# Performance work log

Measured on AMD Instinct MI355X. Metric: run time of the kernel, lower is better.

Reference implementation:

```python
import jax, jax.numpy as jnp
import numpy as np

O, NI, F, D, NN, M = 2048, 16, 4, 128, 8, 8  # outfits, item slots, factors, dim, neighbors, valid slots
D2 = D // 2

def lrelu(x):
    return jax.nn.leaky_relu(x, 0.01)

def mlp2(x, W1, b1, W2, b2):
    # Linear -> LeakyReLU -> Linear -> LeakyReLU (Dropout is identity at inference)
    return lrelu(lrelu(x @ W1 + b1) @ W2 + b2)

def setup_inputs():
    ks = jax.random.split(jax.random.key(0), 16)
    s = 0.05
    pos = jnp.arange(NI)[None, :]
    outfit_items = jnp.where(pos < M, jax.random.randint(ks[0], (O, NI), 0, NI), -1)
    items_neighbor = jax.random.randint(ks[1], (O, NI, NN), -1, NI)
    items_feature = jax.random.normal(ks[2], (O, NI, D), dtype=jnp.float32)
    items_factors = jnp.zeros((O, NI, F, D), dtype=jnp.float32)
    p = {
        'cf_W1': jax.random.normal(ks[3], (F, D, D2)) * s,
        'cf_b1': jnp.zeros((F, D2)),
        'cf_W2': jax.random.normal(ks[4], (F, D2, D)) * s,
        'cf_b2': jnp.zeros((F, D)),
        'f2f_W1': jax.random.normal(ks[5], (D, D)) * s, 'f2f_b1': jnp.zeros((D,)),
        'f2f_W2': jax.random.normal(ks[6], (D, D)) * s, 'f2f_b2': jnp.zeros((D,)),
        'f2i_W1': jax.random.normal(ks[7], (D, D)) * s, 'f2i_b1': jnp.zeros((D,)),
        'f2i_W2': jax.random.normal(ks[8], (D, D)) * s, 'f2i_b2': jnp.zeros((D,)),
        'i2i_W1': jax.random.normal(ks[9], (D, D)) * s, 'i2i_b1': jnp.zeros((D,)),
        'i2i_W2': jax.random.normal(ks[10], (D, D)) * s, 'i2i_b2': jnp.zeros((D,)),
        'o2s_W': jax.random.normal(ks[11], (D, 1)) * s, 'o2s_b': jnp.zeros((1,)),
    }
    return dict(outfit_items=outfit_items, items_feature=items_feature,
                items_neighbor=items_neighbor, items_factors=items_factors, **p)

def _forward(outfit_items, items_feature, items_neighbor, items_factors,
             cf_W1, cf_b1, cf_W2, cf_b2, f2f_W1, f2f_b1, f2f_W2, f2f_b2,
             f2i_W1, f2i_b1, f2i_W2, f2i_b2, i2i_W1, i2i_b1, i2i_W2, i2i_b2,
             o2s_W, o2s_b):
    del items_factors  # creat_factors overwrites every entry in the original
    # --- creat_factors: per-factor 2-layer MLP on every item feature -> [O,NI,F,D]
    h = lrelu(jnp.einsum('oid,fde->oife', items_feature, cf_W1) + cf_b1)
    fac = lrelu(jnp.einsum('oife,fed->oifd', h, cf_W2) + cf_b2)

    # --- inter_factors: sequential over outfit slots; later slots read updated factors
    def outfit_fac(fac_o, oi_o, nbr_o):
        def step(f, i):
            valid = i != -1
            ic = jnp.maximum(i, 0)
            cand = jnp.concatenate([oi_o, nbr_o[ic]])                # [NI+NN]
            cm = (cand != -1) & (cand != i) & valid
            t = f[ic]                                                # [F,D] snapshot
            msg = mlp2(t[None] * f[jnp.maximum(cand, 0)],
                       f2f_W1, f2f_b1, f2f_W2, f2f_b2)               # [NI+NN,F,D]
            add = jnp.sum(jnp.where(cm[:, None, None], msg, 0.0), axis=0)
            return f.at[ic].add(jnp.where(valid, add, 0.0)), None
        f, _ = jax.lax.scan(step, fac_o, oi_o)
        return f
    fac = jax.vmap(outfit_fac)(fac, outfit_items, items_neighbor)

    # --- infer_items: feature[i] += sum_j f2i(fac[i,j]) for outfit members
    g = mlp2(fac, f2i_W1, f2i_b1, f2i_W2, f2i_b2).sum(axis=2)        # [O,NI,D]
    ic = jnp.maximum(outfit_items, 0)
    w = (outfit_items != -1).astype(g.dtype)                          # [O,NI]
    gsel = jnp.take_along_axis(g, ic[..., None], axis=1)
    scat = jax.vmap(lambda gs, idx, ww: jnp.zeros((NI, D), gs.dtype).at[idx].add(ww[:, None] * gs))
    feat = items_feature + scat(gsel, ic, w)

    # --- inter_items: sequential; current value detached (.data in original)
    def outfit_feat(fo_init, oi_o):
        jc = jnp.maximum(oi_o, 0)
        def step(fo, i):
            valid = i != -1
            ic_ = jnp.maximum(i, 0)
            t = jax.lax.stop_gradient(fo[ic_])
            msgs = mlp2(fo[jc], i2i_W1, i2i_b1, i2i_W2, i2i_b2)      # [NI,D]
            m = ((oi_o != -1) & (oi_o != i)).astype(fo.dtype)
            new = t + jnp.sum(m[:, None] * msgs, axis=0)
            return jnp.where(valid, fo.at[ic_].set(new), fo), None
        fo, _ = jax.lax.scan(step, fo_init, oi_o)
        return fo
    feat = jax.vmap(outfit_feat)(feat, outfit_items)

    # --- infer_outfit + score
    fsel = jnp.take_along_axis(feat, ic[..., None], axis=1)
    outfits = jnp.sum(w[..., None] * fsel, axis=1)                    # [O,D]
    scores = jax.nn.sigmoid(outfits @ o2s_W + o2s_b)[:, 0]            # [O]

    # --- com_loss: ||F F^T - I||_F^2 over valid slots (positional mask), / n_outfits
    G = jnp.einsum('oifd,oigd->oifg', fac, fac) - jnp.eye(F, dtype=fac.dtype)
    com = jnp.sum(w * jnp.sum(G * G, axis=(-1, -2))) / O
    return scores, jnp.reshape(com, (1,))

def reference(outfit_items, items_feature, items_neighbor, items_factors,
              cf_W1, cf_b1, cf_W2, cf_b2, f2f_W1, f2f_b1, f2f_W2, f2f_b2,
              f2i_W1, f2i_b1, f2i_W2, f2i_b2, i2i_W1, i2i_b1, i2i_W2, i2i_b2,
              o2s_W, o2s_b):
    return _forward(outfit_items, items_feature, items_neighbor, items_factors,
                    cf_W1, cf_b1, cf_W2, cf_b2, f2f_W1, f2f_b1, f2f_W2, f2f_b2,
                    f2i_W1, f2i_b1, f2i_W2, f2i_b2, i2i_W1, i2i_b1, i2i_W2, i2i_b2,
                    o2s_W, o2s_b)
```

## Files before the change

### kernel.cpp

```cpp
#include <hip/hip_runtime.h>
#include <hip/hip_bf16.h>
#include <math.h>


typedef __attribute__((ext_vector_type(8))) short short8;
typedef __attribute__((ext_vector_type(4))) float f32x4;

#define MFMA16(a, b, c) __builtin_amdgcn_mfma_f32_16x16x32_bf16(a, b, c, 0, 0, 0)

__device__ __forceinline__ float lrelu(float x) { return fmaxf(x, 0.01f * x); }

__device__ __forceinline__ ushort f2bf(float f) {
  unsigned u = __builtin_bit_cast(unsigned, f);
  u += 0x7fffu + ((u >> 16) & 1u);
  return (ushort)(u >> 16);
}
__device__ __forceinline__ float bflo(unsigned u) {
  return __builtin_bit_cast(float, u << 16);
}
__device__ __forceinline__ unsigned pk2(float a, float b) {
  float2 t; t.x = a; t.y = b;
  __hip_bfloat162 h = __float22bfloat162_rn(t);
  unsigned u;
  __builtin_memcpy(&u, &h, 4);
  return u;
}


__global__ __launch_bounds__(256) void prep_weights(
    const float* __restrict__ cfW1, const float* __restrict__ cfW2,
    const float* __restrict__ f2fW1, const float* __restrict__ f2fW2,
    const float* __restrict__ f2iW1, const float* __restrict__ f2iW2,
    const float* __restrict__ i2iW1, const float* __restrict__ i2iW2,
    ushort* __restrict__ ws, float* __restrict__ out) {
  const int idx = (int)(blockIdx.x * 256 + threadIdx.x);
  if (idx == 0) out[2048] = 0.0f;
  float v;
  if (idx < 32768) {
    int f = idx >> 13, r = idx & 8191, n = r >> 7, k = r & 127;
    v = cfW1[f * 8192 + k * 64 + n];
  } else if (idx < 65536) {
    int t = idx - 32768;
    int f = t >> 13, r = t & 8191, n = r >> 6, k = r & 63;
    v = cfW2[f * 8192 + k * 128 + n];
  } else {
    int t = idx - 65536;
    int seg = t >> 14, r = t & 16383, n = r >> 7, k = r & 127;
    const float* W = (seg == 0) ? f2fW1 : (seg == 1) ? f2fW2 :
                     (seg == 2) ? f2iW1 : (seg == 3) ? f2iW2 :
                     (seg == 4) ? i2iW1 : i2iW2;
    v = W[k * 128 + n];
  }
  ws[idx] = f2bf(v);
}

__global__ __launch_bounds__(512, 2) void mfgn_kernel(
    const int* __restrict__ outfit_items,
    const float* __restrict__ items_feature,
    const int* __restrict__ items_neighbor,
    const float* __restrict__ cfb1, const float* __restrict__ cfb2,
    const float* __restrict__ f2fb1, const float* __restrict__ f2fb2,
    const float* __restrict__ f2ib1, const float* __restrict__ f2ib2,
    const float* __restrict__ i2ib1, const float* __restrict__ i2ib2,
    const float* __restrict__ o2sW, const float* __restrict__ o2sb,
    const ushort* __restrict__ wsW,
    float* __restrict__ out)
{
  __shared__ float facL[16 * 540];
  __shared__ ushort prodS[8192] __attribute__((aligned(16)));
  __shared__ ushort hidS[8192] __attribute__((aligned(16)));
  __shared__ ushort featB[2048] __attribute__((aligned(16)));
  __shared__ float redE[8];
  __shared__ int oiL[16];
  __shared__ int clAll[256];
  __shared__ int ncAll[16];
  __shared__ int vslL[16];
  __shared__ int refcntL[16];
  __shared__ int nvsL;

  const int o = blockIdx.x;
  const int tid = (int)threadIdx.x;
  const int lane = tid & 63;
  const int wid = tid >> 6;
  const int n16 = lane & 15;
  const int q = lane >> 4;
  const int kb = q * 8;
  const int col = wid * 16 + n16;
  const int lx = lane * 8;
  const int fS = lane & 3, ciS = lane >> 2;
  const int kc0 = wid * 16;
  const int q0 = (wid & 1) * 2;
  const int sWA = ((wid >> 1) * 4 + (lane >> 4)) * 512 + (lane & 15) * 8;
  const int hwB = (wid >> 1) * 2048 + ((wid & 1) * 2 + (q >> 1)) * 128 + n16 * 8 + (q & 1) * 4;
  const int fbCol = (col >> 5) * 512 + ((col >> 3) & 3) * 128 + (col & 7);

  if (tid < 16) oiL[tid] = outfit_items[o * 16 + tid];
  {
    const int n = tid >> 5, d0 = (tid & 31) * 4;
    float4 v = *(const float4*)(items_feature + o * 2048 + tid * 4);
    uint2 pk; pk.x = pk2(v.x, v.y); pk.y = pk2(v.z, v.w);
    *(uint2*)(featB + (d0 >> 5) * 512 + (((d0 >> 3) & 3) * 16 + n) * 8 + (d0 & 7)) = pk;
  }
  if (tid == 0) {
    int cnt = 0;
    for (int s = 0; s < 16; ++s) refcntL[s] = 0;
    for (int s = 0; s < 16; ++s) {
      int v = oiL[s];
      if (v != -1) { vslL[cnt++] = s; refcntL[v]++; }
    }
    nvsL = cnt;
  }
  for (int s = wid; s < 16; s += 8) {
    const int iv = outfit_items[o * 16 + s];
    if (iv == -1) { if (lane == 0) ncAll[s] = 0; continue; }
    int cand = -1;
    if (lane < 24) cand = (lane < 16) ? outfit_items[o * 16 + lane]
                                      : items_neighbor[o * 128 + iv * 8 + (lane - 16)];
    bool ok = (lane < 24) && (cand != -1) && (cand != iv);
    unsigned long long bm = __ballot(ok);
    if (ok) clAll[s * 16 + __popcll(bm & ((1ull << lane) - 1ull))] = cand;
    if (lane == 0) ncAll[s] = (int)__popcll(bm);
  }
  __syncthreads();
  const int nvs = nvsL;

  {
    const int f = wid & 3, half = wid >> 2;
    short8 wA[2][4];
#pragma unroll
    for (int etl = 0; etl < 2; ++etl)
#pragma unroll
      for (int kt = 0; kt < 4; ++kt)
        wA[etl][kt] = *(const short8*)(wsW + (f * 64 + (half * 2 + etl) * 16 + n16) * 128
                                       + kt * 32 + kb);
    f32x4 acc[2];
#pragma unroll
    for (int etl = 0; etl < 2; ++etl)
      acc[etl] = *(const f32x4*)(cfb1 + f * 64 + (half * 2 + etl) * 16 + q * 4);
    __builtin_amdgcn_s_setprio(1);
    for (int kt = 0; kt < 4; ++kt) {
      short8 x = *(const short8*)(featB + kt * 512 + lx);
      acc[0] = MFMA16(wA[0][kt], x, acc[0]);
      acc[1] = MFMA16(wA[1][kt], x, acc[1]);
    }
    __builtin_amdgcn_s_setprio(0);
#pragma unroll
    for (int etl = 0; etl < 2; ++etl) {
      float h0 = lrelu(acc[etl][0]), h1 = lrelu(acc[etl][1]);
      float h2 = lrelu(acc[etl][2]), h3 = lrelu(acc[etl][3]);
      uint2 pk; pk.x = pk2(h0, h1); pk.y = pk2(h2, h3);
      *(uint2*)(hidS + half * 2048 + f * 512 + (etl * 2 + (q >> 1)) * 128
                + n16 * 8 + (q & 1) * 4) = pk;
    }
    __syncthreads();
    short8 wB[4][2];
#pragma unroll
    for (int ctl = 0; ctl < 4; ++ctl)
#pragma unroll
      for (int kt = 0; kt < 2; ++kt)
        wB[ctl][kt] = *(const short8*)(wsW + 32768 + (f * 128 + half * 64 + ctl * 16 + n16) * 64
                                       + kt * 32 + kb);
    f32x4 acc2[4];
#pragma unroll
    for (int ctl = 0; ctl < 4; ++ctl) {
      float b2 = cfb2[f * 128 + half * 64 + ctl * 16 + n16];
      acc2[ctl] = (f32x4){b2, b2, b2, b2};
    }
    __builtin_amdgcn_s_setprio(1);
    for (int kt = 0; kt < 2; ++kt) {
      short8 h = *(const short8*)(hidS + (kt * 4 + f) * 512 + lx);
#pragma unroll
      for (int ctl = 0; ctl < 4; ++ctl) acc2[ctl] = MFMA16(h, wB[ctl][kt], acc2[ctl]);
    }
    __builtin_amdgcn_s_setprio(0);
#pragma unroll
    for (int ctl = 0; ctl < 4; ++ctl) {
      int c = half * 64 + ctl * 16 + n16;
#pragma unroll
      for (int r = 0; r < 4; ++r)
        facL[(q * 4 + r) * 540 + f * 132 + c] = lrelu(acc2[ctl][r]);
    }
    __syncthreads();
  }

  {
    short8 w1f[4], w2f[4];
#pragma unroll
    for (int kt = 0; kt < 4; ++kt) {
      w1f[kt] = *(const short8*)(wsW + 65536 + col * 128 + kt * 32 + kb);
      w2f[kt] = *(const short8*)(wsW + 81920 + col * 128 + kt * 32 + kb);
    }
    const f32x4 b1q = *(const f32x4*)(f2fb1 + wid * 16 + q * 4);
    const float b2v = f2fb2[col];

    auto stageB = [&](int s, int iv_, int nc_) {
      if (ciS < nc_) {
        const int cit = clAll[s * 16 + ciS];
        const float* tp = facL + iv_ * 540 + fS * 132 + kc0;
        const float* cp = facL + cit * 540 + fS * 132 + kc0;
#pragma unroll
        for (int g = 0; g < 2; ++g) {
          float4 a0 = *(const float4*)(tp + g * 8), a1 = *(const float4*)(tp + g * 8 + 4);
          float4 c0 = *(const float4*)(cp + g * 8), c1 = *(const float4*)(cp + g * 8 + 4);
          uint4 u4;
          u4.x = pk2(a0.x * c0.x, a0.y * c0.y); u4.y = pk2(a0.z * c0.z, a0.w * c0.w);
          u4.z = pk2(a1.x * c1.x, a1.y * c1.y); u4.w = pk2(a1.z * c1.z, a1.w * c1.w);
          *(uint4*)(prodS + sWA + (q0 + g) * 128) = u4;
        }
      }
    };
    auto stageC = [&]() {
      const float* sp = facL + ciS * 540 + fS * 132 + kc0;
#pragma unroll
      for (int g = 0; g < 2; ++g) {
        float4 a0 = *(const float4*)(sp + g * 8), a1 = *(const float4*)(sp + g * 8 + 4);
        uint4 u4;
        u4.x = pk2(a0.x, a0.y); u4.y = pk2(a0.z, a0.w);
        u4.z = pk2(a1.x, a1.y); u4.w = pk2(a1.z, a1.w);
        *(uint4*)(prodS + sWA + (q0 + g) * 128) = u4;
      }
    };

    if (nvs > 0) { const int s0 = vslL[0]; stageB(s0, oiL[s0], ncAll[s0]); }
    __syncthreads();

    for (int u = 0; u < nvs; ++u) {
      const int s = vslL[u];
      const int iv = oiL[s];
      const int nc = ncAll[s];
      f32x4 acc[4];
#pragma unroll
      for (int mt = 0; mt < 4; ++mt) acc[mt] = b1q;
      __builtin_amdgcn_s_setprio(1);
      for (int kt = 0; kt < 4; ++kt)
#pragma unroll
        for (int mt = 0; mt < 4; ++mt) {
          short8 x = *(const short8*)(prodS + (kt * 4 + mt) * 512 + lx);
          acc[mt] = MFMA16(w1f[kt], x, acc[mt]);
        }
      __builtin_amdgcn_s_setprio(0);
#pragma unroll
      for (int mt = 0; mt < 4; ++mt) {
        float h0 = lrelu(acc[mt][0]), h1 = lrelu(acc[mt][1]);
        float h2 = lrelu(acc[mt][2]), h3 = lrelu(acc[mt][3]);
        uint2 pk; pk.x = pk2(h0, h1); pk.y = pk2(h2, h3);
        *(uint2*)(hidS + hwB + mt * 512) = pk;
      }
      __syncthreads();
      f32x4 acc2[4];
#pragma unroll
      for (int mt = 0; mt < 4; ++mt) acc2[mt] = (f32x4){b2v, b2v, b2v, b2v};
      __builtin_amdgcn_s_setprio(1);
      for (int kt = 0; kt < 4; ++kt)
#pragma unroll
        for (int mt = 0; mt < 4; ++mt) {
          short8 h = *(const short8*)(hidS + (kt * 4 + mt) * 512 + lx);
          acc2[mt] = MFMA16(h, w2f[kt], acc2[mt]);
        }
      __builtin_amdgcn_s_setprio(0);
      float part[4] = {0.f, 0.f, 0.f, 0.f};
#pragma unroll
      for (int mt = 0; mt < 4; ++mt) {
        bool act = (mt * 4 + q) < nc;
        if (act) {
#pragma unroll
          for (int r = 0; r < 4; ++r) part[r] += lrelu(acc2[mt][r]);
        }
      }
#pragma unroll
      for (int r = 0; r < 4; ++r) {
        float v = part[r];
        v += __shfl_xor(v, 16);
        v += __shfl_xor(v, 32);
        part[r] = v;
      }
      if (q == 0) {
#pragma unroll
        for (int r = 0; r < 4; ++r)
          facL[iv * 540 + r * 132 + col] += part[r];
      }
      if (u + 1 < nvs) {
        const int s2 = vslL[u + 1];
        stageB(s2, oiL[s2], ncAll[s2]);
      } else {
        stageC();
      }
      __syncthreads();
    }
    if (nvs == 0) { stageC(); __syncthreads(); }
  }

  {
    short8 w1f[4], w2f[4];
#pragma unroll
    for (int kt = 0; kt < 4; ++kt) {
      w1f[kt] = *(const short8*)(wsW + 98304 + col * 128 + kt * 32 + kb);
      w2f[kt] = *(const short8*)(wsW + 114688 + col * 128 + kt * 32 + kb);
    }
    const f32x4 b1q = *(const f32x4*)(f2ib1 + wid * 16 + q * 4);
    const float b2v = f2ib2[col];
    f32x4 acc[4];
#pragma unroll
    for (int mt = 0; mt < 4; ++mt) acc[mt] = b1q;
    __builtin_amdgcn_s_setprio(1);
    for (int kt = 0; kt < 4; ++kt)
#pragma unroll
      for (int mt = 0; mt < 4; ++mt) {
        short8 x = *(const short8*)(prodS + (kt * 4 + mt) * 512 + lx);
        acc[mt] = MFMA16(w1f[kt], x, acc[mt]);
      }
    __builtin_amdgcn_s_setprio(0);
#pragma unroll
    for (int mt = 0; mt < 4; ++mt) {
      float h0 = lrelu(acc[mt][0]), h1 = lrelu(acc[mt][1]);
      float h2 = lrelu(acc[mt][2]), h3 = lrelu(acc[mt][3]);
      uint2 pk; pk.x = pk2(h0, h1); pk.y = pk2(h2, h3);
      *(uint2*)(hidS + hwB + mt * 512) = pk;
    }
    __syncthreads();
    f32x4 acc2[4];
#pragma unroll
    for (int mt = 0; mt < 4; ++mt) acc2[mt] = (f32x4){b2v, b2v, b2v, b2v};
    __builtin_amdgcn_s_setprio(1);
    for (int kt = 0; kt < 4; ++kt)
#pragma unroll
      for (int mt = 0; mt < 4; ++mt) {
        short8 h = *(const short8*)(hidS + (kt * 4 + mt) * 512 + lx);
        acc2[mt] = MFMA16(h, w2f[kt], acc2[mt]);
      }
    __builtin_amdgcn_s_setprio(0);
#pragma unroll
    for (int mt = 0; mt < 4; ++mt) {
      int item = mt * 4 + q;
      float g = 0.f;
#pragma unroll
      for (int r = 0; r < 4; ++r) g += lrelu(acc2[mt][r]);
      int a = fbCol + item * 8;
      featB[a] = f2bf(bflo((unsigned)featB[a]) + (float)refcntL[item] * g);
    }
    __syncthreads();
  }

  {
    short8 w1f[4], w2f[4];
#pragma unroll
    for (int kt = 0; kt < 4; ++kt) {
      w1f[kt] = *(const short8*)(wsW + 131072 + col * 128 + kt * 32 + kb);
      w2f[kt] = *(const short8*)(wsW + 147456 + col * 128 + kt * 32 + kb);
    }
    const f32x4 b1q = *(const f32x4*)(i2ib1 + wid * 16 + q * 4);
    const float b2v = i2ib2[col];
    short8 xc[4];
#pragma unroll
    for (int kt = 0; kt < 4; ++kt)
      xc[kt] = *(const short8*)(featB + kt * 512 + lx);

    for (int u = 0; u < nvs; ++u) {
      const int iv = oiL[vslL[u]];
      f32x4 acc = b1q;
      __builtin_amdgcn_s_setprio(1);
      for (int kt = 0; kt < 4; ++kt) acc = MFMA16(w1f[kt], xc[kt], acc);
      __builtin_amdgcn_s_setprio(0);
      {
        float h0 = lrelu(acc[0]), h1 = lrelu(acc[1]);
        float h2 = lrelu(acc[2]), h3 = lrelu(acc[3]);
        uint2 pk; pk.x = pk2(h0, h1); pk.y = pk2(h2, h3);
        *(uint2*)(hidS + hwB) = pk;
      }
      __syncthreads();
      f32x4 acc2 = (f32x4){b2v, b2v, b2v, b2v};
      __builtin_amdgcn_s_setprio(1);
      for (int kt = 0; kt < 4; ++kt) {
        short8 h = *(const short8*)(hidS + kt * 2048 + lx);
        acc2 = MFMA16(h, w2f[kt], acc2);
      }
      __builtin_amdgcn_s_setprio(0);
      float part = 0.f;
#pragma unroll
      for (int r = 0; r < 4; ++r) {
        int item = q * 4 + r;
        float w = (item == iv) ? 0.0f : (float)refcntL[item];
        part += w * lrelu(acc2[r]);
      }
      part += __shfl_xor(part, 16);
      part += __shfl_xor(part, 32);
      if (q == 0) {
        int a = fbCol + iv * 8;
        featB[a] = f2bf(bflo((unsigned)featB[a]) + part);
      }
      __syncthreads();
      if (n16 == iv) {
#pragma unroll
        for (int kt = 0; kt < 4; ++kt)
          xc[kt] = *(const short8*)(featB + kt * 512 + lx);
      }
    }
  }

  if (tid < 128) {
    const int eb = (tid >> 5) * 512 + ((tid >> 3) & 3) * 128 + (tid & 7);
    float sum = 0.0f;
    for (int u = 0; u < nvs; ++u) {
      int it = oiL[vslL[u]];
      sum += bflo((unsigned)featB[eb + it * 8]);
    }
    float v = sum * o2sW[tid];
#pragma unroll
    for (int off = 1; off < 64; off <<= 1) v += __shfl_xor(v, off);
    if (lane == 0) redE[wid] = v;
  }
  __syncthreads();
  if (tid == 0) {
    float t = redE[0] + redE[1] + o2sb[0];
    out[o] = 1.0f / (1.0f + expf(-t));
  }

  {
    const int n = tid >> 5, f = (tid >> 3) & 3, g = (tid >> 1) & 3, h = tid & 1;
    float dot = 0.0f;
    if (f <= g) {
      const float* pa = facL + n * 540 + f * 132 + h * 64;
      const float* pb = facL + n * 540 + g * 132 + h * 64;
      for (int i = 0; i < 16; ++i) {
        float4 a = *(const float4*)(pa + i * 4);
        float4 b = *(const float4*)(pb + i * 4);
        dot += a.x * b.x + a.y * b.y + a.z * b.z + a.w * b.w;
      }
    }
    dot += __shfl_xor(dot, 1);
    float v = dot - ((f == g) ? 1.0f : 0.0f);
    float wgt = (f == g) ? 1.0f : 2.0f;
    float sq = (h == 0 && f <= g && oiL[n] != -1) ? wgt * v * v : 0.0f;
#pragma unroll
    for (int off = 1; off < 64; off <<= 1) sq += __shfl_xor(sq, off);
    __syncthreads();
    if (lane == 0) redE[wid] = sq;
    __syncthreads();
    if (tid == 0) {
      float tot = 0.f;
#pragma unroll
      for (int w = 0; w < 8; ++w) tot += redE[w];
      atomicAdd(out + 2048, tot * (1.0f / 2048.0f));
    }
  }
}

extern "C" void kernel_launch(void* const* d_in, const int* in_sizes, int n_in,
                              void* d_out, int out_size, void* d_ws, size_t ws_size,
                              hipStream_t stream) {
  float* out = (float*)d_out;
  ushort* ws = (ushort*)d_ws;
  hipLaunchKernelGGL(prep_weights, dim3(640), dim3(256), 0, stream,
                     (const float*)d_in[4], (const float*)d_in[6],
                     (const float*)d_in[8], (const float*)d_in[10],
                     (const float*)d_in[12], (const float*)d_in[14],
                     (const float*)d_in[16], (const float*)d_in[18],
                     ws, out);
  hipLaunchKernelGGL(mfgn_kernel, dim3(2048), dim3(512), 0, stream,
                     (const int*)d_in[0],
                     (const float*)d_in[1],
                     (const int*)d_in[2],
                     (const float*)d_in[5], (const float*)d_in[7],
                     (const float*)d_in[9], (const float*)d_in[11],
                     (const float*)d_in[13], (const float*)d_in[15],
                     (const float*)d_in[17], (const float*)d_in[19],
                     (const float*)d_in[20], (const float*)d_in[21],
                     (const ushort*)ws,
                     out);
}
```

Baseline: 316.7 us.

## Shrink LDS and registers to fit three 512-thread blocks per CU

Merges the prodS and hidS shared buffers into one bufS, removes padding from the facL row stride and narrows the index arrays to bytes, all to cut LDS use per block. It also loads the second-layer weights just before use rather than up front, lowering register pressure, and raises launch bounds from 2 to 3 blocks per CU. Sharing one buffer needs extra __syncthreads barriers, and the unpadded facL stride may bring back LDS bank conflicts.

```diff
diff --git a/kernel.cpp b/kernel.cpp
--- a/kernel.cpp
+++ b/kernel.cpp
@@ -54,7 +54,7 @@
   ws[idx] = f2bf(v);
 }
 
-__global__ __launch_bounds__(512, 2) void mfgn_kernel(
+__global__ __launch_bounds__(512, 3) void mfgn_kernel(
     const int* __restrict__ outfit_items,
     const float* __restrict__ items_feature,
     const int* __restrict__ items_neighbor,
@@ -66,16 +66,15 @@
     const ushort* __restrict__ wsW,
     float* __restrict__ out)
 {
-  __shared__ float facL[16 * 540];
-  __shared__ ushort prodS[8192] __attribute__((aligned(16)));
-  __shared__ ushort hidS[8192] __attribute__((aligned(16)));
+  __shared__ float facL[16 * 516];
+  __shared__ ushort bufS[8192] __attribute__((aligned(16)));
   __shared__ ushort featB[2048] __attribute__((aligned(16)));
   __shared__ float redE[8];
-  __shared__ int oiL[16];
-  __shared__ int clAll[256];
-  __shared__ int ncAll[16];
-  __shared__ int vslL[16];
-  __shared__ int refcntL[16];
+  __shared__ signed char oiL[16];
+  __shared__ unsigned char clAllU[256];
+  __shared__ unsigned char ncAll[16];
+  __shared__ unsigned char vslL[16];
+  __shared__ unsigned char refcntL[16];
   __shared__ int nvsL;
 
   const int o = blockIdx.x;
@@ -94,7 +93,7 @@
   const int hwB = (wid >> 1) * 2048 + ((wid & 1) * 2 + (q >> 1)) * 128 + n16 * 8 + (q & 1) * 4;
   const int fbCol = (col >> 5) * 512 + ((col >> 3) & 3) * 128 + (col & 7);
 
-  if (tid < 16) oiL[tid] = outfit_items[o * 16 + tid];
+  if (tid < 16) oiL[tid] = (signed char)outfit_items[o * 16 + tid];
   {
     const int n = tid >> 5, d0 = (tid & 31) * 4;
     float4 v = *(const float4*)(items_feature + o * 2048 + tid * 4);
@@ -103,11 +102,13 @@
   }
   if (tid == 0) {
     int cnt = 0;
-    for (int s = 0; s < 16; ++s) refcntL[s] = 0;
+    int rc[16];
+    for (int s = 0; s < 16; ++s) rc[s] = 0;
     for (int s = 0; s < 16; ++s) {
-      int v = oiL[s];
-      if (v != -1) { vslL[cnt++] = s; refcntL[v]++; }
-    }
+      int v = (int)oiL[s];
+      if (v != -1) { vslL[cnt++] = (unsigned char)s; rc[v]++; }
+    }
+    for (int s = 0; s < 16; ++s) refcntL[s] = (unsigned char)rc[s];
     nvsL = cnt;
   }
   for (int s = wid; s < 16; s += 8) {
@@ -118,8 +119,8 @@
                                       : items_neighbor[o * 128 + iv * 8 + (lane - 16)];
     bool ok = (lane < 24) && (cand != -1) && (cand != iv);
     unsigned long long bm = __ballot(ok);
-    if (ok) clAll[s * 16 + __popcll(bm & ((1ull << lane) - 1ull))] = cand;
-    if (lane == 0) ncAll[s] = (int)__popcll(bm);
+    if (ok) clAllU[s * 16 + __popcll(bm & ((1ull << lane) - 1ull))] = (unsigned char)cand;
+    if (lane == 0) ncAll[s] = (unsigned char)__popcll(bm);
   }
   __syncthreads();
   const int nvs = nvsL;
@@ -149,7 +150,7 @@
       float h0 = lrelu(acc[etl][0]), h1 = lrelu(acc[etl][1]);
       float h2 = lrelu(acc[etl][2]), h3 = lrelu(acc[etl][3]);
       uint2 pk; pk.x = pk2(h0, h1); pk.y = pk2(h2, h3);
-      *(uint2*)(hidS + half * 2048 + f * 512 + (etl * 2 + (q >> 1)) * 128
+      *(uint2*)(bufS + half * 2048 + f * 512 + (etl * 2 + (q >> 1)) * 128
                 + n16 * 8 + (q & 1) * 4) = pk;
     }
     __syncthreads();
@@ -168,7 +169,7 @@
     }
     __builtin_amdgcn_s_setprio(1);
     for (int kt = 0; kt < 2; ++kt) {
-      short8 h = *(const short8*)(hidS + (kt * 4 + f) * 512 + lx);
+      short8 h = *(const short8*)(bufS + (kt * 4 + f) * 512 + lx);
 #pragma unroll
       for (int ctl = 0; ctl < 4; ++ctl) acc2[ctl] = MFMA16(h, wB[ctl][kt], acc2[ctl]);
     }
@@ -178,26 +179,24 @@
       int c = half * 64 + ctl * 16 + n16;
 #pragma unroll
       for (int r = 0; r < 4; ++r)
-        facL[(q * 4 + r) * 540 + f * 132 + c] = lrelu(acc2[ctl][r]);
-    }
-    __syncthreads();
-  }
-
-  {
-    short8 w1f[4], w2f[4];
-#pragma unroll
-    for (int kt = 0; kt < 4; ++kt) {
+        facL[(q * 4 + r) * 516 + f * 128 + c] = lrelu(acc2[ctl][r]);
+    }
+    __syncthreads();
+  }
+
+  {
+    short8 w1f[4];
+#pragma unroll
+    for (int kt = 0; kt < 4; ++kt)
       w1f[kt] = *(const short8*)(wsW + 65536 + col * 128 + kt * 32 + kb);
-      w2f[kt] = *(const short8*)(wsW + 81920 + col * 128 + kt * 32 + kb);
-    }
     const f32x4 b1q = *(const f32x4*)(f2fb1 + wid * 16 + q * 4);
     const float b2v = f2fb2[col];
 
     auto stageB = [&](int s, int iv_, int nc_) {
       if (ciS < nc_) {
-        const int cit = clAll[s * 16 + ciS];
-        const float* tp = facL + iv_ * 540 + fS * 132 + kc0;
-        const float* cp = facL + cit * 540 + fS * 132 + kc0;
+        const int cit = (int)clAllU[s * 16 + ciS];
+        const float* tp = facL + iv_ * 516 + fS * 128 + kc0;
+        const float* cp = facL + cit * 516 + fS * 128 + kc0;
 #pragma unroll
         for (int g = 0; g < 2; ++g) {
           float4 a0 = *(const float4*)(tp + g * 8), a1 = *(const float4*)(tp + g * 8 + 4);
@@ -205,29 +204,29 @@
           uint4 u4;
           u4.x = pk2(a0.x * c0.x, a0.y * c0.y); u4.y = pk2(a0.z * c0.z, a0.w * c0.w);
           u4.z = pk2(a1.x * c1.x, a1.y * c1.y); u4.w = pk2(a1.z * c1.z, a1.w * c1.w);
-          *(uint4*)(prodS + sWA + (q0 + g) * 128) = u4;
+          *(uint4*)(bufS + sWA + (q0 + g) * 128) = u4;
         }
       }
     };
     auto stageC = [&]() {
-      const float* sp = facL + ciS * 540 + fS * 132 + kc0;
+      const float* sp = facL + ciS * 516 + fS * 128 + kc0;
 #pragma unroll
       for (int g = 0; g < 2; ++g) {
         float4 a0 = *(const float4*)(sp + g * 8), a1 = *(const float4*)(sp + g * 8 + 4);
         uint4 u4;
         u4.x = pk2(a0.x, a0.y); u4.y = pk2(a0.z, a0.w);
         u4.z = pk2(a1.x, a1.y); u4.w = pk2(a1.z, a1.w);
-        *(uint4*)(prodS + sWA + (q0 + g) * 128) = u4;
+        *(uint4*)(bufS + sWA + (q0 + g) * 128) = u4;
       }
     };
 
-    if (nvs > 0) { const int s0 = vslL[0]; stageB(s0, oiL[s0], ncAll[s0]); }
+    if (nvs > 0) { const int s0 = vslL[0]; stageB(s0, (int)oiL[s0], (int)ncAll[s0]); }
     __syncthreads();
 
     for (int u = 0; u < nvs; ++u) {
-      const int s = vslL[u];
-      const int iv = oiL[s];
-      const int nc = ncAll[s];
+      const int s = (int)vslL[u];
+      const int iv = (int)oiL[s];
+      const int nc = (int)ncAll[s];
       f32x4 acc[4];
 #pragma unroll
       for (int mt = 0; mt < 4; ++mt) acc[mt] = b1q;
@@ -235,16 +234,21 @@
       for (int kt = 0; kt < 4; ++kt)
 #pragma unroll
         for (int mt = 0; mt < 4; ++mt) {
-          short8 x = *(const short8*)(prodS + (kt * 4 + mt) * 512 + lx);
+          short8 x = *(const short8*)(bufS + (kt * 4 + mt) * 512 + lx);
           acc[mt] = MFMA16(w1f[kt], x, acc[mt]);
         }
       __builtin_amdgcn_s_setprio(0);
+      short8 w2f[4];
+#pragma unroll
+      for (int kt = 0; kt < 4; ++kt)
+        w2f[kt] = *(const short8*)(wsW + 81920 + col * 128 + kt * 32 + kb);
+      __syncthreads();
 #pragma unroll
       for (int mt = 0; mt < 4; ++mt) {
         float h0 = lrelu(acc[mt][0]), h1 = lrelu(acc[mt][1]);
         float h2 = lrelu(acc[mt][2]), h3 = lrelu(acc[mt][3]);
         uint2 pk; pk.x = pk2(h0, h1); pk.y = pk2(h2, h3);
-        *(uint2*)(hidS + hwB + mt * 512) = pk;
+        *(uint2*)(bufS + hwB + mt * 512) = pk;
       }
       __syncthreads();
       f32x4 acc2[4];
@@ -254,7 +258,7 @@
       for (int kt = 0; kt < 4; ++kt)
 #pragma unroll
         for (int mt = 0; mt < 4; ++mt) {
-          short8 h = *(const short8*)(hidS + (kt * 4 + mt) * 512 + lx);
+          short8 h = *(const short8*)(bufS + (kt * 4 + mt) * 512 + lx);
           acc2[mt] = MFMA16(h, w2f[kt], acc2[mt]);
         }
       __builtin_amdgcn_s_setprio(0);
@@ -277,11 +281,12 @@
       if (q == 0) {
 #pragma unroll
         for (int r = 0; r < 4; ++r)
-          facL[iv * 540 + r * 132 + col] += part[r];
-      }
+          facL[iv * 516 + r * 128 + col] += part[r];
+      }
+      __syncthreads();
       if (u + 1 < nvs) {
-        const int s2 = vslL[u + 1];
-        stageB(s2, oiL[s2], ncAll[s2]);
+        const int s2 = (int)vslL[u + 1];
+        stageB(s2, (int)oiL[s2], (int)ncAll[s2]);
       } else {
         stageC();
       }
@@ -291,12 +296,10 @@
   }
 
   {
-    short8 w1f[4], w2f[4];
-#pragma unroll
-    for (int kt = 0; kt < 4; ++kt) {
+    short8 w1f[4];
+#pragma unroll
+    for (int kt = 0; kt < 4; ++kt)
       w1f[kt] = *(const short8*)(wsW + 98304 + col * 128 + kt * 32 + kb);
-      w2f[kt] = *(const short8*)(wsW + 114688 + col * 128 + kt * 32 + kb);
-    }
     const f32x4 b1q = *(const f32x4*)(f2ib1 + wid * 16 + q * 4);
     const float b2v = f2ib2[col];
     f32x4 acc[4];
@@ -306,16 +309,21 @@
     for (int kt = 0; kt < 4; ++kt)
 #pragma unroll
       for (int mt = 0; mt < 4; ++mt) {
-        short8 x = *(const short8*)(prodS + (kt * 4 + mt) * 512 + lx);
+        short8 x = *(const short8*)(bufS + (kt * 4 + mt) * 512 + lx);
         acc[mt] = MFMA16(w1f[kt], x, acc[mt]);
       }
     __builtin_amdgcn_s_setprio(0);
+    short8 w2f[4];
+#pragma unroll
+    for (int kt = 0; kt < 4; ++kt)
+      w2f[kt] = *(const short8*)(wsW + 114688 + col * 128 + kt * 32 + kb);
+    __syncthreads();
 #pragma unroll
     for (int mt = 0; mt < 4; ++mt) {
       float h0 = lrelu(acc[mt][0]), h1 = lrelu(acc[mt][1]);
       float h2 = lrelu(acc[mt][2]), h3 = lrelu(acc[mt][3]);
       uint2 pk; pk.x = pk2(h0, h1); pk.y = pk2(h2, h3);
-      *(uint2*)(hidS + hwB + mt * 512) = pk;
+      *(uint2*)(bufS + hwB + mt * 512) = pk;
     }
     __syncthreads();
     f32x4 acc2[4];
@@ -325,7 +333,7 @@
     for (int kt = 0; kt < 4; ++kt)
 #pragma unroll
       for (int mt = 0; mt < 4; ++mt) {
-        short8 h = *(const short8*)(hidS + (kt * 4 + mt) * 512 + lx);
+        short8 h = *(const short8*)(bufS + (kt * 4 + mt) * 512 + lx);
         acc2[mt] = MFMA16(h, w2f[kt], acc2[mt]);
       }
     __builtin_amdgcn_s_setprio(0);
@@ -342,12 +350,10 @@
   }
 
   {
-    short8 w1f[4], w2f[4];
-#pragma unroll
-    for (int kt = 0; kt < 4; ++kt) {
+    short8 w1f[4];
+#pragma unroll
+    for (int kt = 0; kt < 4; ++kt)
       w1f[kt] = *(const short8*)(wsW + 131072 + col * 128 + kt * 32 + kb);
-      w2f[kt] = *(const short8*)(wsW + 147456 + col * 128 + kt * 32 + kb);
-    }
     const f32x4 b1q = *(const f32x4*)(i2ib1 + wid * 16 + q * 4);
     const float b2v = i2ib2[col];
     short8 xc[4];
@@ -356,22 +362,26 @@
       xc[kt] = *(const short8*)(featB + kt * 512 + lx);
 
     for (int u = 0; u < nvs; ++u) {
-      const int iv = oiL[vslL[u]];
+      const int iv = (int)oiL[(int)vslL[u]];
       f32x4 acc = b1q;
       __builtin_amdgcn_s_setprio(1);
       for (int kt = 0; kt < 4; ++kt) acc = MFMA16(w1f[kt], xc[kt], acc);
       __builtin_amdgcn_s_setprio(0);
+      short8 w2f[4];
+#pragma unroll
+      for (int kt = 0; kt < 4; ++kt)
+        w2f[kt] = *(const short8*)(wsW + 147456 + col * 128 + kt * 32 + kb);
       {
         float h0 = lrelu(acc[0]), h1 = lrelu(acc[1]);
         float h2 = lrelu(acc[2]), h3 = lrelu(acc[3]);
         uint2 pk; pk.x = pk2(h0, h1); pk.y = pk2(h2, h3);
-        *(uint2*)(hidS + hwB) = pk;
+        *(uint2*)(bufS + hwB) = pk;
       }
       __syncthreads();
       f32x4 acc2 = (f32x4){b2v, b2v, b2v, b2v};
       __builtin_amdgcn_s_setprio(1);
       for (int kt = 0; kt < 4; ++kt) {
-        short8 h = *(const short8*)(hidS + kt * 2048 + lx);
+        short8 h = *(const short8*)(bufS + kt * 2048 + lx);
         acc2 = MFMA16(h, w2f[kt], acc2);
       }
       __builtin_amdgcn_s_setprio(0);
@@ -401,7 +411,7 @@
     const int eb = (tid >> 5) * 512 + ((tid >> 3) & 3) * 128 + (tid & 7);
     float sum = 0.0f;
     for (int u = 0; u < nvs; ++u) {
-      int it = oiL[vslL[u]];
+      int it = (int)oiL[(int)vslL[u]];
       sum += bflo((unsigned)featB[eb + it * 8]);
     }
     float v = sum * o2sW[tid];
@@ -419,8 +429,8 @@
     const int n = tid >> 5, f = (tid >> 3) & 3, g = (tid >> 1) & 3, h = tid & 1;
     float dot = 0.0f;
     if (f <= g) {
-      const float* pa = facL + n * 540 + f * 132 + h * 64;
-      const float* pb = facL + n * 540 + g * 132 + h * 64;
+      const float* pa = facL + n * 516 + f * 128 + h * 64;
+      const float* pb = facL + n * 516 + g * 128 + h * 64;
       for (int i = 0; i < 16; ++i) {
         float4 a = *(const float4*)(pa + i * 4);
         float4 b = *(const float4*)(pb + i * 4);
```

Measured after the change: 349.1 us. 10.2% more time.
